# Kernel tuning notes

Measured on AMD Instinct MI355X. Metric: run time of the kernel, lower is better.

Reference implementation:

```python
import jax, jax.numpy as jnp
import numpy as np

E = 1024
H = 16
D = E // H  # head_dim = 64
B, L, S = 2, 2048, 2048


def setup_inputs() -> dict:
    key = jax.random.key(0)
    ks = jax.random.split(key, 10)
    scale = 1.0 / np.sqrt(E)
    return {
        "x": jax.random.normal(ks[0], (B, L, E), jnp.float32),
        "context": jax.random.normal(ks[1], (B, S, E), jnp.float32),
        "Wq": jax.random.normal(ks[2], (E, E), jnp.float32) * scale,
        "bq": jnp.zeros((E,), jnp.float32),
        "Wk": jax.random.normal(ks[3], (E, E), jnp.float32) * scale,
        "bk": jnp.zeros((E,), jnp.float32),
        "Wv": jax.random.normal(ks[4], (E, E), jnp.float32) * scale,
        "bv": jnp.zeros((E,), jnp.float32),
        "Wp": jax.random.normal(ks[5], (E, E), jnp.float32) * scale,
        "bp": jnp.zeros((E,), jnp.float32),
    }


def reference(x, context, Wq, bq, Wk, bk, Wv, bv, Wp, bp):
    b, l, _ = x.shape
    s = context.shape[1]
    # linear projections then split heads: [B, H, L/S, D]
    q = (x @ Wq + bq).reshape(b, l, H, D).transpose(0, 2, 1, 3)
    k = (context @ Wk + bk).reshape(b, s, H, D).transpose(0, 2, 1, 3)
    v = (context @ Wv + bv).reshape(b, s, H, D).transpose(0, 2, 1, 3)
    # scores [B, H, L, S]
    attn = jnp.einsum("bhld,bhsd->bhls", q, k) / jnp.sqrt(jnp.float32(D))
    attn = jax.nn.softmax(attn, axis=-1)
    # dropout is identity in eval mode
    out = jnp.einsum("bhls,bhsd->bhld", attn, v)
    out = out.transpose(0, 2, 1, 3).reshape(b, l, E)
    return out @ Wp + bp
```

## Files before the change

### kernel.cpp

```cpp
#include <hip/hip_runtime.h>
#include <math.h>

#define B_ 2
#define L_ 2048
#define S_ 2048
#define E_ 1024
#define H_ 16
#define D_ 64
#define SC_ 0.180336880111120f

typedef unsigned short u16;
typedef unsigned int u32;
typedef __attribute__((ext_vector_type(8))) short short8;
typedef __attribute__((ext_vector_type(4))) float floatx4;

__device__ __forceinline__ u16 f2bf(float f) {
    union { float f; unsigned u; } a; a.f = f;
    unsigned r = a.u + 0x7FFFu + ((a.u >> 16) & 1u);
    return (u16)(r >> 16);
}

__device__ __forceinline__ u32 cvt_pk_bf16(float lo, float hi) {
    u32 d;
    asm("v_cvt_pk_bf16_f32 %0, %1, %2" : "=v"(d) : "v"(lo), "v"(hi));
    return d;
}

__device__ __forceinline__ void glds16(const u16* g, u16* l) {
    __builtin_amdgcn_global_load_lds(
        (const __attribute__((address_space(1))) void*)g,
        (__attribute__((address_space(3))) void*)l, 16, 0, 0);
}

__global__ void cast_bf16_kernel(const float* __restrict__ x, const float* __restrict__ ctx,
                                 u16* __restrict__ Xb, u16* __restrict__ Cb) {
    const float* src = blockIdx.y ? ctx : x;
    u16* dst = blockIdx.y ? Cb : Xb;
    int i = blockIdx.x * 256 + threadIdx.x;
    float4 u0 = ((const float4*)src)[2 * i];
    float4 u1 = ((const float4*)src)[2 * i + 1];
    uint4 o;
    o.x = cvt_pk_bf16(u0.x, u0.y);
    o.y = cvt_pk_bf16(u0.z, u0.w);
    o.z = cvt_pk_bf16(u1.x, u1.y);
    o.w = cvt_pk_bf16(u1.z, u1.w);
    ((uint4*)dst)[i] = o;
}

__global__ void transpose_cast_kernel(const float* __restrict__ Wq, const float* __restrict__ Wk,
                                      const float* __restrict__ Wv, const float* __restrict__ Wp,
                                      u16* __restrict__ WqT, u16* __restrict__ WkT,
                                      u16* __restrict__ WvT, u16* __restrict__ WpT) {
    const int z = blockIdx.z;
    const float* W = z == 0 ? Wq : (z == 1 ? Wk : (z == 2 ? Wv : Wp));
    u16* Wt = z == 0 ? WqT : (z == 1 ? WkT : (z == 2 ? WvT : WpT));
    __shared__ float tile[32][33];
    const int bx = blockIdx.x * 32, by = blockIdx.y * 32;
    const int tx = threadIdx.x, ty = threadIdx.y;
#pragma unroll
    for (int j = 0; j < 4; ++j)
        tile[ty + j * 8][tx] = W[(size_t)(by + ty + j * 8) * E_ + bx + tx];
    __syncthreads();
#pragma unroll
    for (int j = 0; j < 4; ++j)
        Wt[(size_t)(bx + ty + j * 8) * E_ + by + tx] = f2bf(tile[tx][ty + j * 8]);
}

__device__ __forceinline__ void xcd_remap(int bx, int by, int& m_idx, int& n_idx) {
    int lin = bx + 8 * by;
    int c8 = lin & 7;
    int g = lin >> 3;
    m_idx = c8 + 8 * (g & 3);
    n_idx = g >> 2;
}

__global__ __launch_bounds__(256, 2) void qkv_gemm_kernel(
    const u16* __restrict__ Xb, const u16* __restrict__ Cb,
    const u16* __restrict__ WqT, const u16* __restrict__ WkT, const u16* __restrict__ WvT,
    const float* __restrict__ bq, const float* __restrict__ bk, const float* __restrict__ bv,
    u16* __restrict__ Qb, u16* __restrict__ Kb, u16* __restrict__ Vtb) {
    __shared__ __align__(16) u16 As[2][128 * 64];
    __shared__ __align__(16) u16 Bs[2][128 * 64];

    const int z = blockIdx.z;
    const u16* A  = z == 0 ? Xb : Cb;
    const u16* Bt = z == 0 ? WqT : (z == 1 ? WkT : WvT);
    const float* bias = z == 0 ? bq : (z == 1 ? bk : bv);
    const float scale = z == 0 ? SC_ : 1.0f;

    const int tid = threadIdx.x;
    const int lane = tid & 63;
    const int wv = tid >> 6;
    const int wm = wv >> 1, wn = wv & 1;
    const int qd = lane >> 4, lr = lane & 15;
    int m_idx, n_idx;
    xcd_remap(blockIdx.x, blockIdx.y, m_idx, n_idx);
    const int m0 = m_idx * 128, n0 = n_idx * 128;
    const int lrow = lane >> 3;
    const int gu = (lane & 7) ^ lrow;

    floatx4 acc[4][4];
#pragma unroll
    for (int i = 0; i < 4; ++i)
#pragma unroll
        for (int j = 0; j < 4; ++j) {
            floatx4 zz = {0.f, 0.f, 0.f, 0.f};
            acc[i][j] = zz;
        }

#define STAGE_AB(buf, kb)                                                          \
    {                                                                              \
        _Pragma("unroll") for (int j = 0; j < 4; ++j) {                            \
            int c = wv * 4 + j;                                                    \
            glds16(A + (size_t)(m0 + c * 8 + lrow) * E_ + (kb) + gu * 8,           \
                   &As[buf][c * 512]);                                             \
            glds16(Bt + (size_t)(n0 + c * 8 + lrow) * E_ + (kb) + gu * 8,          \
                   &Bs[buf][c * 512]);                                             \
        }                                                                          \
    }

    STAGE_AB(0, 0)
    __syncthreads();

    for (int t = 0; t < 16; ++t) {
        const int cur = t & 1;
        if (t + 1 < 16) STAGE_AB(cur ^ 1, (t + 1) * 64)

        short8 af[4][2], bf[4][2];
#pragma unroll
        for (int mi = 0; mi < 4; ++mi)
#pragma unroll
            for (int kk = 0; kk < 2; ++kk) {
                int row = wm * 64 + mi * 16 + lr;
                int u = (kk * 4 + qd) ^ (lr & 7);
                af[mi][kk] = *(const short8*)(&As[cur][row * 64 + u * 8]);
            }
#pragma unroll
        for (int ni = 0; ni < 4; ++ni)
#pragma unroll
            for (int kk = 0; kk < 2; ++kk) {
                int row = wn * 64 + ni * 16 + lr;
                int u = (kk * 4 + qd) ^ (lr & 7);
                bf[ni][kk] = *(const short8*)(&Bs[cur][row * 64 + u * 8]);
            }
#pragma unroll
        for (int kk = 0; kk < 2; ++kk)
#pragma unroll
            for (int mi = 0; mi < 4; ++mi)
#pragma unroll
                for (int ni = 0; ni < 4; ++ni)
                    acc[mi][ni] = __builtin_amdgcn_mfma_f32_16x16x32_bf16(
                        af[mi][kk], bf[ni][kk], acc[mi][ni], 0, 0, 0);

        __syncthreads();
    }

    u16* Cq = z == 0 ? Qb : Kb;
#pragma unroll
    for (int mi = 0; mi < 4; ++mi) {
#pragma unroll
        for (int ni = 0; ni < 4; ++ni) {
            int col = n0 + wn * 64 + ni * 16 + lr;
            float bv_ = bias[col];
            if (z == 2) {
                int row0 = m0 + wm * 64 + mi * 16 + qd * 4;
                int bidx = row0 >> 11;
                int sloc = row0 & (S_ - 1);
                u16 h0 = f2bf(acc[mi][ni][0] + bv_);
                u16 h1 = f2bf(acc[mi][ni][1] + bv_);
                u16 h2 = f2bf(acc[mi][ni][2] + bv_);
                u16 h3 = f2bf(acc[mi][ni][3] + bv_);
                uint2 pk;
                pk.x = h0 | ((unsigned)h1 << 16);
                pk.y = h2 | ((unsigned)h3 << 16);
                *(uint2*)&Vtb[((size_t)(bidx * E_ + col)) * S_ + sloc] = pk;
            } else {
#pragma unroll
                for (int r = 0; r < 4; ++r) {
                    int row = m0 + wm * 64 + mi * 16 + qd * 4 + r;
                    Cq[(size_t)row * E_ + col] = f2bf((acc[mi][ni][r] + bv_) * scale);
                }
            }
        }
    }
#undef STAGE_AB
}

#define PSTR 68

__global__ __launch_bounds__(256, 3) void flash_attn_kernel(
    const u16* __restrict__ Q, const u16* __restrict__ Kg,
    const u16* __restrict__ Vtg, u16* __restrict__ Opart, float* __restrict__ lpart) {
    __shared__ __align__(16) u16 Ps[128 * PSTR];
    __shared__ __align__(16) u16 Ks[2][64 * 64];
    __shared__ __align__(16) u16 Vs[2][64 * 64];

    const int tid = threadIdx.x;
    const int lane = tid & 63;
    const int wv = tid >> 6;
    const int qd = lane >> 4, lr = lane & 15;
    const int b = blockIdx.y >> 4, h = blockIdx.y & 15;
    const int q0 = blockIdx.x * 128;
    const int z = blockIdx.z;
    const int sbeg = z * (S_ / 2);

    u16* Op = Opart + (size_t)z * (B_ * L_ * E_);
    float* lp = lpart + (size_t)z * (B_ * H_ * L_);

    const u16* Qbase = Q + (size_t)(b * L_ + q0) * E_ + h * D_;
    const u16* Kbase = Kg + (size_t)(b * S_) * E_ + h * D_;
    const u16* Vbase = Vtg + (size_t)(b * E_ + h * D_) * S_;

    const int srow = tid >> 3;
    const int scol = (tid & 7) * 8;
    const int lrow = lane >> 3;
    const int gu = (lane & 7) ^ lrow;

#pragma unroll
    for (int j = 0; j < 2; ++j) {
        int c = wv * 2 + j;
        glds16(Kbase + (size_t)(sbeg + c * 8 + lrow) * E_ + gu * 8, &Ks[0][c * 512]);
        glds16(Vbase + (size_t)(c * 8 + lrow) * S_ + sbeg + gu * 8, &Vs[0][c * 512]);
    }

#pragma unroll
    for (int c = 0; c < 4; ++c) {
        int row = srow + c * 32;
        *(uint4*)(&Ps[row * PSTR + scol]) = *(const uint4*)(Qbase + (size_t)row * E_ + scol);
    }
    __syncthreads();

    short8 qf[2][2];
#pragma unroll
    for (int mi = 0; mi < 2; ++mi)
#pragma unroll
        for (int kk = 0; kk < 2; ++kk)
            qf[mi][kk] = *(const short8*)(&Ps[(wv * 32 + mi * 16 + lr) * PSTR + kk * 32 + qd * 8]);

    floatx4 o_acc[2][4];
    float l_acc[2][4];
#pragma unroll
    for (int mi = 0; mi < 2; ++mi)
#pragma unroll
        for (int nt = 0; nt < 4; ++nt) {
            floatx4 z4 = {0.f, 0.f, 0.f, 0.f};
            o_acc[mi][nt] = z4;
        }
#pragma unroll
    for (int mi = 0; mi < 2; ++mi)
#pragma unroll
        for (int r = 0; r < 4; ++r) l_acc[mi][r] = 0.f;

    const int NIT = (S_ / 2) / 64;

    for (int it = 0; it < NIT; ++it) {
        const int cur = it & 1;
        if (it + 1 < NIT) {
            int s1 = sbeg + (it + 1) * 64;
#pragma unroll
            for (int j = 0; j < 2; ++j) {
                int c = wv * 2 + j;
                glds16(Kbase + (size_t)(s1 + c * 8 + lrow) * E_ + gu * 8, &Ks[cur ^ 1][c * 512]);
                glds16(Vbase + (size_t)(c * 8 + lrow) * S_ + s1 + gu * 8, &Vs[cur ^ 1][c * 512]);
            }
        }

        floatx4 s_[2][4];
#pragma unroll
        for (int nt = 0; nt < 4; ++nt) {
            int krow = nt * 16 + lr;
            short8 kb0 = *(const short8*)(&Ks[cur][krow * 64 + ((qd) ^ (lr & 7)) * 8]);
            short8 kb1 = *(const short8*)(&Ks[cur][krow * 64 + ((4 + qd) ^ (lr & 7)) * 8]);
#pragma unroll
            for (int mi = 0; mi < 2; ++mi) {
                floatx4 zz = {0.f, 0.f, 0.f, 0.f};
                zz = __builtin_amdgcn_mfma_f32_16x16x32_bf16(qf[mi][0], kb0, zz, 0, 0, 0);
                zz = __builtin_amdgcn_mfma_f32_16x16x32_bf16(qf[mi][1], kb1, zz, 0, 0, 0);
                s_[mi][nt] = zz;
            }
        }

#pragma unroll
        for (int mi = 0; mi < 2; ++mi)
#pragma unroll
            for (int nt = 0; nt < 4; ++nt)
#pragma unroll
                for (int r = 0; r < 4; ++r) {
                    float p = __builtin_amdgcn_exp2f(s_[mi][nt][r]);
                    l_acc[mi][r] += p;
                    Ps[(wv * 32 + mi * 16 + qd * 4 + r) * PSTR + nt * 16 + lr] = f2bf(p);
                }
        asm volatile("s_waitcnt lgkmcnt(0)" ::: "memory");

        short8 pf[2][2];
#pragma unroll
        for (int mi = 0; mi < 2; ++mi)
#pragma unroll
            for (int kk = 0; kk < 2; ++kk)
                pf[mi][kk] = *(const short8*)(&Ps[(wv * 32 + mi * 16 + lr) * PSTR + kk * 32 + qd * 8]);
#pragma unroll
        for (int nt = 0; nt < 4; ++nt) {
            int vrow = nt * 16 + lr;
            short8 vb0 = *(const short8*)(&Vs[cur][vrow * 64 + ((qd) ^ (lr & 7)) * 8]);
            short8 vb1 = *(const short8*)(&Vs[cur][vrow * 64 + ((4 + qd) ^ (lr & 7)) * 8]);
#pragma unroll
            for (int mi = 0; mi < 2; ++mi) {
                o_acc[mi][nt] = __builtin_amdgcn_mfma_f32_16x16x32_bf16(pf[mi][0], vb0, o_acc[mi][nt], 0, 0, 0);
                o_acc[mi][nt] = __builtin_amdgcn_mfma_f32_16x16x32_bf16(pf[mi][1], vb1, o_acc[mi][nt], 0, 0, 0);
            }
        }

        __syncthreads();
    }

    float linv[2][4];
#pragma unroll
    for (int mi = 0; mi < 2; ++mi)
#pragma unroll
        for (int r = 0; r < 4; ++r) {
            float l = l_acc[mi][r];
#pragma unroll
            for (int st = 1; st < 16; st <<= 1) l += __shfl_xor(l, st);
            if (lr == 0)
                lp[(size_t)(b * H_ + h) * L_ + q0 + wv * 32 + mi * 16 + qd * 4 + r] = l;
            linv[mi][r] = 1.0f / l;
        }

#pragma unroll
    for (int mi = 0; mi < 2; ++mi)
#pragma unroll
        for (int nt = 0; nt < 4; ++nt)
#pragma unroll
            for (int r = 0; r < 4; ++r) {
                int row = q0 + wv * 32 + mi * 16 + qd * 4 + r;
                int col = h * D_ + nt * 16 + lr;
                Op[(size_t)(b * L_ + row) * E_ + col] = f2bf(o_acc[mi][nt][r] * linv[mi][r]);
            }
}

__global__ __launch_bounds__(256, 2) void out_gemm_kernel(
    const u16* __restrict__ O1, const u16* __restrict__ O2,
    const float* __restrict__ l1, const float* __restrict__ l2,
    const u16* __restrict__ WpT, const float* __restrict__ bp,
    float* __restrict__ out) {
    __shared__ __align__(16) u16 As[2][128 * 64];
    __shared__ __align__(16) u16 Bs[2][128 * 64];

    const int tid = threadIdx.x;
    const int lane = tid & 63;
    const int wv = tid >> 6;
    const int wm = wv >> 1, wn = wv & 1;
    const int qd = lane >> 4, lr = lane & 15;
    int m_idx, n_idx;
    xcd_remap(blockIdx.x, blockIdx.y, m_idx, n_idx);
    const int m0 = m_idx * 128, n0 = n_idx * 128;
    const int lrow = lane >> 3;
    const int gu = (lane & 7) ^ lrow;

    floatx4 acc[4][4];
#pragma unroll
    for (int i = 0; i < 4; ++i)
#pragma unroll
        for (int j = 0; j < 4; ++j) {
            floatx4 zz = {0.f, 0.f, 0.f, 0.f};
            acc[i][j] = zz;
        }

    uint4 p1[4], p2[4];
    float la_[4], lb_[4];

#define LOAD_AO(tt)                                                                \
    {                                                                              \
        _Pragma("unroll") for (int j = 0; j < 4; ++j) {                            \
            int c = wv * 4 + j;                                                    \
            int row = m0 + c * 8 + lrow;                                           \
            int col = (tt)*64 + gu * 8;                                            \
            p1[j] = *(const uint4*)(O1 + (size_t)row * E_ + col);                  \
            p2[j] = *(const uint4*)(O2 + (size_t)row * E_ + col);                  \
            int li = (row >> 11) * (H_ * L_) + (tt)*L_ + (row & (L_ - 1));         \
            la_[j] = l1[li];                                                       \
            lb_[j] = l2[li];                                                       \
        }                                                                          \
    }

#define WRITE_AO(buf)                                                              \
    {                                                                              \
        _Pragma("unroll") for (int j = 0; j < 4; ++j) {                            \
            int c = wv * 4 + j;                                                    \
            float s = 1.0f / (la_[j] + lb_[j]);                                    \
            float w1 = la_[j] * s, w2 = lb_[j] * s;                                \
            const u32* pa = (const u32*)&p1[j];                                    \
            const u32* pb = (const u32*)&p2[j];                                    \
            uint4 o;                                                               \
            u32* po = (u32*)&o;                                                    \
            _Pragma("unroll") for (int d = 0; d < 4; ++d) {                        \
                union { u32 u; float f; } x0, x1, y0, y1;                          \
                x0.u = pa[d] << 16; x1.u = pa[d] & 0xFFFF0000u;                    \
                y0.u = pb[d] << 16; y1.u = pb[d] & 0xFFFF0000u;                    \
                po[d] = cvt_pk_bf16(x0.f * w1 + y0.f * w2, x1.f * w1 + y1.f * w2); \
            }                                                                      \
            *(uint4*)(&As[buf][c * 512 + lane * 8]) = o;                           \
        }                                                                          \
    }

#define STAGE_BO(buf, kb)                                                          \
    {                                                                              \
        _Pragma("unroll") for (int j = 0; j < 4; ++j) {                            \
            int c = wv * 4 + j;                                                    \
            glds16(WpT + (size_t)(n0 + c * 8 + lrow) * E_ + (kb) + gu * 8,         \
                   &Bs[buf][c * 512]);                                             \
        }                                                                          \
    }

    LOAD_AO(0)
    STAGE_BO(0, 0)
    WRITE_AO(0)
    __syncthreads();

    for (int t = 0; t < 16; ++t) {
        const int cur = t & 1;
        if (t + 1 < 16) {
            STAGE_BO(cur ^ 1, (t + 1) * 64)
            LOAD_AO(t + 1)
        }

        short8 af[4][2], bf[4][2];
#pragma unroll
        for (int mi = 0; mi < 4; ++mi)
#pragma unroll
            for (int kk = 0; kk < 2; ++kk) {
                int row = wm * 64 + mi * 16 + lr;
                int u = (kk * 4 + qd) ^ (lr & 7);
                af[mi][kk] = *(const short8*)(&As[cur][row * 64 + u * 8]);
            }
#pragma unroll
        for (int ni = 0; ni < 4; ++ni)
#pragma unroll
            for (int kk = 0; kk < 2; ++kk) {
                int row = wn * 64 + ni * 16 + lr;
                int u = (kk * 4 + qd) ^ (lr & 7);
                bf[ni][kk] = *(const short8*)(&Bs[cur][row * 64 + u * 8]);
            }
#pragma unroll
        for (int kk = 0; kk < 2; ++kk)
#pragma unroll
            for (int mi = 0; mi < 4; ++mi)
#pragma unroll
                for (int ni = 0; ni < 4; ++ni)
                    acc[mi][ni] = __builtin_amdgcn_mfma_f32_16x16x32_bf16(
                        af[mi][kk], bf[ni][kk], acc[mi][ni], 0, 0, 0);

        if (t + 1 < 16) WRITE_AO(cur ^ 1)
        __syncthreads();
    }

#pragma unroll
    for (int mi = 0; mi < 4; ++mi)
#pragma unroll
        for (int ni = 0; ni < 4; ++ni) {
            int col = n0 + wn * 64 + ni * 16 + lr;
            float bv_ = bp[col];
#pragma unroll
            for (int r = 0; r < 4; ++r) {
                int row = m0 + wm * 64 + mi * 16 + qd * 4 + r;
                out[(size_t)row * E_ + col] = acc[mi][ni][r] + bv_;
            }
        }
#undef LOAD_AO
#undef WRITE_AO
#undef STAGE_BO
}

extern "C" void kernel_launch(void* const* d_in, const int* in_sizes, int n_in,
                              void* d_out, int out_size, void* d_ws, size_t ws_size,
                              hipStream_t stream) {
    const float* x   = (const float*)d_in[0];
    const float* ctx = (const float*)d_in[1];
    const float* Wq  = (const float*)d_in[2];
    const float* bq  = (const float*)d_in[3];
    const float* Wk  = (const float*)d_in[4];
    const float* bk  = (const float*)d_in[5];
    const float* Wv  = (const float*)d_in[6];
    const float* bv  = (const float*)d_in[7];
    const float* Wp  = (const float*)d_in[8];
    const float* bp  = (const float*)d_in[9];
    float* out = (float*)d_out;

    u16* WqT = (u16*)d_ws;
    u16* WkT = WqT + 1048576;
    u16* WvT = WkT + 1048576;
    u16* WpT = WvT + 1048576;
    u16* Qb  = WpT + 1048576;
    u16* Kb  = Qb + 4194304;
    u16* Vtb = Kb + 4194304;
    u16* Xb  = Vtb + 4194304;
    u16* Cb  = Xb + 4194304;
    u16* Opart = Xb;
    float* lpart = (float*)(Cb + 4194304);
    (void)ws_size; (void)in_sizes; (void)n_in; (void)out_size;

    cast_bf16_kernel<<<dim3(2048, 2), 256, 0, stream>>>(x, ctx, Xb, Cb);
    transpose_cast_kernel<<<dim3(32, 32, 4), dim3(32, 8), 0, stream>>>(
        Wq, Wk, Wv, Wp, WqT, WkT, WvT, WpT);

    qkv_gemm_kernel<<<dim3(8, 32, 3), 256, 0, stream>>>(
        Xb, Cb, WqT, WkT, WvT, bq, bk, bv, Qb, Kb, Vtb);

    flash_attn_kernel<<<dim3(L_ / 128, B_ * H_, 2), 256, 0, stream>>>(
        Qb, Kb, Vtb, Opart, lpart);

    out_gemm_kernel<<<dim3(8, 32), 256, 0, stream>>>(
        Opart, Opart + 4194304, lpart, lpart + B_ * H_ * L_, WpT, bp, out);
}
```

Before: 239.7 us.

## Keep softmax probabilities in registers via transposed QK and permlane swaps

Computes S transposed (K as A operand) so each lane holds probabilities along the key dimension. Packs them to bf16 and rearranges them with v_permlane32/16_swap into the A-operand layout for the PV MFMA, removing the LDS round trip for P. Q fragments are now loaded straight from global memory, the row sum becomes a per-lane scalar reduced with two shuffles, and occupancy is raised to 4 blocks since LDS use drops. The risk is that the swap mapping must exactly match the MFMA operand layout, and the uncoalesced global Q loads add some cost.

```diff
diff --git a/kernel.cpp b/kernel.cpp
--- a/kernel.cpp
+++ b/kernel.cpp
@@ -24,6 +24,13 @@
     u32 d;
     asm("v_cvt_pk_bf16_f32 %0, %1, %2" : "=v"(d) : "v"(lo), "v"(hi));
     return d;
+}
+
+__device__ __forceinline__ void pl32swap(u32& a, u32& b) {
+    asm("v_permlane32_swap_b32 %0, %1" : "+v"(a), "+v"(b));
+}
+__device__ __forceinline__ void pl16swap(u32& a, u32& b) {
+    asm("v_permlane16_swap_b32 %0, %1" : "+v"(a), "+v"(b));
 }
 
 __device__ __forceinline__ void glds16(const u16* g, u16* l) {
@@ -186,12 +193,9 @@
 #undef STAGE_AB
 }
 
-#define PSTR 68
-
-__global__ __launch_bounds__(256, 3) void flash_attn_kernel(
+__global__ __launch_bounds__(256, 4) void flash_attn_kernel(
     const u16* __restrict__ Q, const u16* __restrict__ Kg,
     const u16* __restrict__ Vtg, u16* __restrict__ Opart, float* __restrict__ lpart) {
-    __shared__ __align__(16) u16 Ps[128 * PSTR];
     __shared__ __align__(16) u16 Ks[2][64 * 64];
     __shared__ __align__(16) u16 Vs[2][64 * 64];
 
@@ -207,12 +211,9 @@
     u16* Op = Opart + (size_t)z * (B_ * L_ * E_);
     float* lp = lpart + (size_t)z * (B_ * H_ * L_);
 
-    const u16* Qbase = Q + (size_t)(b * L_ + q0) * E_ + h * D_;
     const u16* Kbase = Kg + (size_t)(b * S_) * E_ + h * D_;
     const u16* Vbase = Vtg + (size_t)(b * E_ + h * D_) * S_;
 
-    const int srow = tid >> 3;
-    const int scol = (tid & 7) * 8;
     const int lrow = lane >> 3;
     const int gu = (lane & 7) ^ lrow;
 
@@ -223,22 +224,16 @@
         glds16(Vbase + (size_t)(c * 8 + lrow) * S_ + sbeg + gu * 8, &Vs[0][c * 512]);
     }
 
-#pragma unroll
-    for (int c = 0; c < 4; ++c) {
-        int row = srow + c * 32;
-        *(uint4*)(&Ps[row * PSTR + scol]) = *(const uint4*)(Qbase + (size_t)row * E_ + scol);
-    }
-    __syncthreads();
-
     short8 qf[2][2];
 #pragma unroll
     for (int mi = 0; mi < 2; ++mi)
 #pragma unroll
         for (int kk = 0; kk < 2; ++kk)
-            qf[mi][kk] = *(const short8*)(&Ps[(wv * 32 + mi * 16 + lr) * PSTR + kk * 32 + qd * 8]);
+            qf[mi][kk] = *(const short8*)(Q + (size_t)(b * L_ + q0 + wv * 32 + mi * 16 + lr) * E_ +
+                                          h * D_ + kk * 32 + qd * 8);
 
     floatx4 o_acc[2][4];
-    float l_acc[2][4];
+    float l_acc[2] = {0.f, 0.f};
 #pragma unroll
     for (int mi = 0; mi < 2; ++mi)
 #pragma unroll
@@ -246,10 +241,8 @@
             floatx4 z4 = {0.f, 0.f, 0.f, 0.f};
             o_acc[mi][nt] = z4;
         }
-#pragma unroll
-    for (int mi = 0; mi < 2; ++mi)
-#pragma unroll
-        for (int r = 0; r < 4; ++r) l_acc[mi][r] = 0.f;
+
+    __syncthreads();
 
     const int NIT = (S_ / 2) / 64;
 
@@ -274,30 +267,42 @@
 #pragma unroll
             for (int mi = 0; mi < 2; ++mi) {
                 floatx4 zz = {0.f, 0.f, 0.f, 0.f};
-                zz = __builtin_amdgcn_mfma_f32_16x16x32_bf16(qf[mi][0], kb0, zz, 0, 0, 0);
-                zz = __builtin_amdgcn_mfma_f32_16x16x32_bf16(qf[mi][1], kb1, zz, 0, 0, 0);
+                zz = __builtin_amdgcn_mfma_f32_16x16x32_bf16(kb0, qf[mi][0], zz, 0, 0, 0);
+                zz = __builtin_amdgcn_mfma_f32_16x16x32_bf16(kb1, qf[mi][1], zz, 0, 0, 0);
                 s_[mi][nt] = zz;
             }
         }
 
-#pragma unroll
-        for (int mi = 0; mi < 2; ++mi)
-#pragma unroll
-            for (int nt = 0; nt < 4; ++nt)
-#pragma unroll
-                for (int r = 0; r < 4; ++r) {
-                    float p = __builtin_amdgcn_exp2f(s_[mi][nt][r]);
-                    l_acc[mi][r] += p;
-                    Ps[(wv * 32 + mi * 16 + qd * 4 + r) * PSTR + nt * 16 + lr] = f2bf(p);
-                }
-        asm volatile("s_waitcnt lgkmcnt(0)" ::: "memory");
-
         short8 pf[2][2];
 #pragma unroll
-        for (int mi = 0; mi < 2; ++mi)
-#pragma unroll
-            for (int kk = 0; kk < 2; ++kk)
-                pf[mi][kk] = *(const short8*)(&Ps[(wv * 32 + mi * 16 + lr) * PSTR + kk * 32 + qd * 8]);
+        for (int mi = 0; mi < 2; ++mi) {
+            u32 dg[4][2];
+            float ls = 0.f;
+#pragma unroll
+            for (int nt = 0; nt < 4; ++nt) {
+                float p0 = __builtin_amdgcn_exp2f(s_[mi][nt][0]);
+                float p1 = __builtin_amdgcn_exp2f(s_[mi][nt][1]);
+                float p2 = __builtin_amdgcn_exp2f(s_[mi][nt][2]);
+                float p3 = __builtin_amdgcn_exp2f(s_[mi][nt][3]);
+                ls += (p0 + p1) + (p2 + p3);
+                dg[nt][0] = cvt_pk_bf16(p0, p1);
+                dg[nt][1] = cvt_pk_bf16(p2, p3);
+            }
+            l_acc[mi] += ls;
+#pragma unroll
+            for (int kk = 0; kk < 2; ++kk) {
+                u32 x0 = dg[2 * kk][0], y0 = dg[2 * kk + 1][0];
+                pl32swap(x0, y0);
+                pl16swap(x0, y0);
+                u32 x1 = dg[2 * kk][1], y1 = dg[2 * kk + 1][1];
+                pl32swap(x1, y1);
+                pl16swap(x1, y1);
+                union { u32 d[4]; short8 v; } u;
+                u.d[0] = x0; u.d[1] = x1; u.d[2] = y0; u.d[3] = y1;
+                pf[mi][kk] = u.v;
+            }
+        }
+
 #pragma unroll
         for (int nt = 0; nt < 4; ++nt) {
             int vrow = nt * 16 + lr;
@@ -315,16 +320,16 @@
 
     float linv[2][4];
 #pragma unroll
-    for (int mi = 0; mi < 2; ++mi)
-#pragma unroll
-        for (int r = 0; r < 4; ++r) {
-            float l = l_acc[mi][r];
-#pragma unroll
-            for (int st = 1; st < 16; st <<= 1) l += __shfl_xor(l, st);
-            if (lr == 0)
-                lp[(size_t)(b * H_ + h) * L_ + q0 + wv * 32 + mi * 16 + qd * 4 + r] = l;
-            linv[mi][r] = 1.0f / l;
-        }
+    for (int mi = 0; mi < 2; ++mi) {
+        float l = l_acc[mi];
+        l += __shfl_xor(l, 16);
+        l += __shfl_xor(l, 32);
+        if (lane < 16)
+            lp[(size_t)(b * H_ + h) * L_ + q0 + wv * 32 + mi * 16 + lane] = l;
+        float il = 1.0f / l;
+#pragma unroll
+        for (int r = 0; r < 4; ++r) linv[mi][r] = __shfl(il, qd * 4 + r);
+    }
 
 #pragma unroll
     for (int mi = 0; mi < 2; ++mi)
```

Measured after the change: 221.5 us. 1.08x faster.
